# Kernel tuning notes

Hardware: AMD Instinct MI355X
Metric: run time of the kernel (lower is better)

The kernel has to match this reference:

```python
import jax, jax.numpy as jnp
import numpy as np

# Multi-scale feature pyramid (H, W) per level: strides 8/16/32/64 on a ~512px image
SHAPES = ((64, 64), (32, 32), (16, 16), (8, 8))
N_HEADS, N_LEVELS, N_POINTS = 8, 4, 4
D_MODEL = 256
HEAD_DIM = D_MODEL // N_HEADS


def setup_inputs() -> dict:
    key = jax.random.key(0)
    ks = jax.random.split(key, 11)
    B, C = 4, D_MODEL
    Lv = sum(h * w for h, w in SHAPES)  # 5440
    Lq = Lv  # encoder self-attention: queries are the flattened features
    scale = 0.02
    return {
        "query": jax.random.normal(ks[0], (B, Lq, C), jnp.float32),
        "reference_points": jax.random.uniform(ks[1], (B, Lq, N_LEVELS, 2), jnp.float32),
        "value": jax.random.normal(ks[2], (B, Lv, C), jnp.float32),
        "W_off": jax.random.normal(ks[3], (C, N_HEADS * N_LEVELS * N_POINTS * 2), jnp.float32) * scale,
        "b_off": jax.random.normal(ks[4], (N_HEADS * N_LEVELS * N_POINTS * 2,), jnp.float32) * 0.5,
        "W_attn": jax.random.normal(ks[5], (C, N_HEADS * N_LEVELS * N_POINTS), jnp.float32) * scale,
        "b_attn": jax.random.normal(ks[6], (N_HEADS * N_LEVELS * N_POINTS,), jnp.float32) * scale,
        "W_val": jax.random.normal(ks[7], (C, C), jnp.float32) * scale,
        "b_val": jax.random.normal(ks[8], (C,), jnp.float32) * scale,
        "W_out": jax.random.normal(ks[9], (C, C), jnp.float32) * scale,
        "b_out": jax.random.normal(ks[10], (C,), jnp.float32) * scale,
    }


def _bilinear_sample(val, grid, H, W):
    """Replicates F.grid_sample(mode='bilinear', padding_mode='zeros', align_corners=False).

    val:  [N, C, H, W]
    grid: [N, Lq, P, 2] in [-1, 1] (x, y order)
    returns: [N, C, Lq, P]
    """
    N, C = val.shape[0], val.shape[1]
    # unnormalize (align_corners=False)
    x = (grid[..., 0] + 1.0) * 0.5 * W - 0.5  # [N, Lq, P]
    y = (grid[..., 1] + 1.0) * 0.5 * H - 0.5
    x0 = jnp.floor(x)
    y0 = jnp.floor(y)
    wx = x - x0  # fractional parts
    wy = y - y0
    flat = val.reshape(N, C, H * W)

    def gather(xi, yi):
        valid = (xi >= 0) & (xi < W) & (yi >= 0) & (yi < H)
        xc = jnp.clip(xi, 0, W - 1).astype(jnp.int32)
        yc = jnp.clip(yi, 0, H - 1).astype(jnp.int32)
        idx = yc * W + xc  # [N, Lq, P]
        g = jax.vmap(lambda v, i: v[:, i])(flat, idx)  # [N, C, Lq, P]
        return g * valid[:, None, :, :].astype(val.dtype)

    out = (gather(x0, y0) * ((1 - wx) * (1 - wy))[:, None]
           + gather(x0 + 1, y0) * (wx * (1 - wy))[:, None]
           + gather(x0, y0 + 1) * ((1 - wx) * wy)[:, None]
           + gather(x0 + 1, y0 + 1) * (wx * wy)[:, None])
    return out


def _ms_deform_attn(query, reference_points, value, W_off, b_off, W_attn, b_attn,
                    W_val, b_val, W_out, b_out):
    B, Lq, C = query.shape
    val = value @ W_val + b_val  # [B, Lv, C]
    val = val.reshape(B, -1, N_HEADS, HEAD_DIM)

    offsets = (query @ W_off + b_off).reshape(B, Lq, N_HEADS, N_LEVELS, N_POINTS, 2)
    weights = jax.nn.softmax(
        (query @ W_attn + b_attn).reshape(B, Lq, N_HEADS, N_LEVELS * N_POINTS), axis=-1
    ).reshape(B, Lq, N_HEADS, N_LEVELS, N_POINTS)

    # offset normalizer: (W, H) per level
    offset_norm = jnp.array([[w, h] for h, w in SHAPES], jnp.float32)
    # ref_dim == 2 branch
    locs = reference_points[:, :, None, :, None, :] + offsets / offset_norm[None, None, None, :, None, :]
    grids = 2.0 * locs - 1.0  # [B, Lq, nh, nl, np, 2]

    acc = jnp.zeros((B * N_HEADS, HEAD_DIM, Lq), query.dtype)
    start = 0
    for lid, (H, W) in enumerate(SHAPES):
        # [B, HW, nh, hd] -> [B*nh, hd, H, W]
        v = val[:, start:start + H * W].transpose(0, 2, 3, 1).reshape(B * N_HEADS, HEAD_DIM, H, W)
        g = grids[:, :, :, lid].transpose(0, 2, 1, 3, 4).reshape(B * N_HEADS, Lq, N_POINTS, 2)
        s = _bilinear_sample(v, g, H, W)  # [B*nh, hd, Lq, np]
        w = weights[:, :, :, lid].transpose(0, 2, 1, 3).reshape(B * N_HEADS, 1, Lq, N_POINTS)
        acc = acc + (s * w).sum(-1)
        start += H * W

    out = acc.reshape(B, D_MODEL, Lq).transpose(0, 2, 1)  # [B, Lq, C]
    return out @ W_out + b_out


def reference(query, reference_points, value, W_off, b_off, W_attn, b_attn,
              W_val, b_val, W_out, b_out):
    return _ms_deform_attn(query, reference_points, value, W_off, b_off,
                           W_attn, b_attn, W_val, b_val, W_out, b_out)
```

## Files before the change

### kernel.cpp

```cpp
#include <hip/hip_runtime.h>


typedef __attribute__((ext_vector_type(8))) _Float16 half8;
typedef __attribute__((ext_vector_type(4))) _Float16 half4;
typedef __attribute__((ext_vector_type(4))) float f32x4;

typedef __attribute__((address_space(3))) unsigned int lds_uint;
typedef const __attribute__((address_space(1))) unsigned int g_uint;

__device__ __forceinline__ void load_lds16(const _Float16* g, _Float16* l) {
    __builtin_amdgcn_global_load_lds((g_uint*)g, (lds_uint*)l, 16, 0, 0);
}

__device__ __forceinline__ half8 splat8(_Float16 v) {
    half8 r = {v, v, v, v, v, v, v, v};
    return r;
}

#define M_TOTAL 21760

__global__ __launch_bounds__(256, 4) void gemm12_cvt(
    const float* __restrict__ value, const float* __restrict__ query,
    const float* __restrict__ W_val, const float* __restrict__ W_off,
    const float* __restrict__ W_attn,
    const float* __restrict__ b_val, const float* __restrict__ b_off,
    const float* __restrict__ b_attn,
    _Float16* __restrict__ valh, _Float16* __restrict__ offh)
{
    __shared__ _Float16 Af[2][4 * 64 * 8];
    __shared__ _Float16 Bf[2][4 * 128 * 8];

    const bool g1 = blockIdx.x < 680;
    const int id = g1 ? blockIdx.x : blockIdx.x - 680;
    const int mt = g1 ? (id >> 1) : (id / 3);
    const int nt = g1 ? (id & 1) : (id % 3);
    const int NN = g1 ? 256 : 384;
    const float* A = g1 ? value : query;
    _Float16* C = g1 ? valh : offh;
    const int bm = mt * 64;
    const int bn = nt * 128;

    const float* W;
    int sW, nb;
    if (g1)            { W = W_val;  sW = 256; nb = bn; }
    else if (nt < 2)   { W = W_off;  sW = 256; nb = bn; }
    else               { W = W_attn; sW = 128; nb = 0;  }

    const int tid = threadIdx.x;
    const int wave = tid >> 6, lane = tid & 63;
    const int wm = (wave & 1) * 32, wn = (wave >> 1) * 64;
    const int ml = lane & 15;
    const int gq = lane >> 4;

    const int ar = tid & 63,  ag = tid >> 6;
    const int bc = tid & 127, bh = tid >> 7;

    const float* aS = A + (size_t)(bm + ar) * 256 + ag * 8;
    const float* wS = W + (size_t)(bh * 16) * sW + nb + bc;

    float4 pa0, pa1;
    float pb[16];

    auto LOAD = [&](int kt) {
        const float* p = aS + kt * 32;
        pa0 = *(const float4*)(p + 0);
        pa1 = *(const float4*)(p + 4);
        const float* q = wS + (size_t)kt * 32 * sW;
#pragma unroll
        for (int e = 0; e < 16; ++e) pb[e] = q[(size_t)e * sW];
    };

    auto WRITE = [&](int buf) {
        const half8 ha = {(_Float16)pa0.x, (_Float16)pa0.y, (_Float16)pa0.z, (_Float16)pa0.w,
                          (_Float16)pa1.x, (_Float16)pa1.y, (_Float16)pa1.z, (_Float16)pa1.w};
        const half8 hb0 = {(_Float16)pb[0], (_Float16)pb[1], (_Float16)pb[2], (_Float16)pb[3],
                           (_Float16)pb[4], (_Float16)pb[5], (_Float16)pb[6], (_Float16)pb[7]};
        const half8 hb1 = {(_Float16)pb[8], (_Float16)pb[9], (_Float16)pb[10], (_Float16)pb[11],
                           (_Float16)pb[12], (_Float16)pb[13], (_Float16)pb[14], (_Float16)pb[15]};
        *(half8*)(&Af[buf][0] + ((ag * 64 + ar) << 3)) = ha;
        *(half8*)(&Bf[buf][0] + (((bh * 2) * 128 + bc) << 3)) = hb0;
        *(half8*)(&Bf[buf][0] + (((bh * 2 + 1) * 128 + bc) << 3)) = hb1;
    };

    const f32x4 zero4 = {0.f, 0.f, 0.f, 0.f};
    f32x4 acc[2][4];
#pragma unroll
    for (int i = 0; i < 2; ++i)
#pragma unroll
        for (int j = 0; j < 4; ++j) acc[i][j] = zero4;

    LOAD(0);
    int cur = 0;
    for (int kt = 0; kt < 8; ++kt) {
        WRITE(cur);
        if (kt < 7) LOAD(kt + 1);
        __syncthreads();

        half8 af[2], bf[4];
        const _Float16* ab = &Af[cur][0] + ((size_t)gq * 64 << 3);
        const _Float16* bb = &Bf[cur][0] + ((size_t)gq * 128 << 3);
#pragma unroll
        for (int i = 0; i < 2; ++i)
            af[i] = *(const half8*)(ab + ((wm + i * 16 + ml) << 3));
#pragma unroll
        for (int j = 0; j < 4; ++j)
            bf[j] = *(const half8*)(bb + ((wn + j * 16 + ml) << 3));
#pragma unroll
        for (int i = 0; i < 2; ++i)
#pragma unroll
            for (int j = 0; j < 4; ++j)
                acc[i][j] = __builtin_amdgcn_mfma_f32_16x16x32_f16(af[i], bf[j], acc[i][j], 0, 0, 0);
        cur ^= 1;
    }

    const int r0 = (lane >> 4) * 4;
#pragma unroll
    for (int j = 0; j < 4; ++j) {
        const int col = bn + wn + j * 16 + ml;
        const float bj = g1 ? b_val[col] : (col < 256 ? b_off[col] : b_attn[col - 256]);
#pragma unroll
        for (int i = 0; i < 2; ++i) {
            const size_t rbase = (size_t)(bm + wm + i * 16 + r0) * NN + col;
#pragma unroll
            for (int r = 0; r < 4; ++r)
                C[rbase + (size_t)r * NN] = (_Float16)(acc[i][j][r] + bj);
        }
    }
}

__device__ __forceinline__ void gemm_core(
    const _Float16* __restrict__ A, const _Float16* __restrict__ Bt,
    const float* __restrict__ bias, float* __restrict__ Cv,
    int NN, int mt, int nt)
{
    __shared__ _Float16 Ah[128 * 32];
    __shared__ _Float16 Bh[64 * 32];

    const int tid = threadIdx.x;
    const int bm = mt * 128;
    const int bn = nt * 64;
    const int wave = tid >> 6, lane = tid & 63;
    const int wm = (wave & 1) * 64, wn = (wave >> 1) * 32;
    const int ml = lane & 15, kq = (lane >> 4) * 8;
    const int lr = lane >> 2;
    const int lk = (lane & 3) * 8;

    const f32x4 zero4 = {0.f, 0.f, 0.f, 0.f};
    f32x4 acc[4][2];
#pragma unroll
    for (int i = 0; i < 4; ++i)
#pragma unroll
        for (int j = 0; j < 2; ++j) acc[i][j] = zero4;

    for (int kt = 0; kt < 8; ++kt) {
        const int k0 = kt * 32;
        __syncthreads();
#pragma unroll
        for (int t = 0; t < 2; ++t) {
            const int row = wave * 32 + t * 16;
            load_lds16(A + (size_t)(bm + row + lr) * 256 + k0 + lk,
                       Ah + (size_t)row * 32);
        }
        {
            const int row = wave * 16;
            load_lds16(Bt + (size_t)(bn + row + lr) * 256 + k0 + lk,
                       Bh + (size_t)row * 32);
        }
        __syncthreads();

        half8 af[4], bf[2];
#pragma unroll
        for (int i = 0; i < 4; ++i)
            af[i] = *(const half8*)(Ah + (wm + i * 16 + ml) * 32 + kq);
#pragma unroll
        for (int j = 0; j < 2; ++j)
            bf[j] = *(const half8*)(Bh + (wn + j * 16 + ml) * 32 + kq);
#pragma unroll
        for (int i = 0; i < 4; ++i)
#pragma unroll
            for (int j = 0; j < 2; ++j)
                acc[i][j] = __builtin_amdgcn_mfma_f32_16x16x32_f16(af[i], bf[j], acc[i][j], 0, 0, 0);
    }

    const int r0 = (lane >> 4) * 4;
#pragma unroll
    for (int j = 0; j < 2; ++j) {
        const int col = bn + wn + j * 16 + ml;
        const float bj = bias[col];
#pragma unroll
        for (int i = 0; i < 4; ++i) {
            const size_t rbase = (size_t)(bm + wm + i * 16 + r0) * NN + col;
#pragma unroll
            for (int r = 0; r < 4; ++r)
                Cv[rbase + (size_t)r * NN] = acc[i][j][r] + bj;
        }
    }
}

__global__ __launch_bounds__(256) void gemm_single(
    const _Float16* __restrict__ A, const _Float16* __restrict__ Bt,
    const float* __restrict__ bias, float* __restrict__ Cv)
{
    const int id = blockIdx.x;
    gemm_core(A, Bt, bias, Cv, 256, id >> 2, id & 3);
}

__global__ __launch_bounds__(256, 4) void sample_f16(
    const _Float16* __restrict__ valh,
    const float* __restrict__ refp,
    const _Float16* __restrict__ offh,
    const float* __restrict__ W_out,
    _Float16* __restrict__ wto,
    _Float16* __restrict__ acc_out)
{
    if (blockIdx.x < 256)
        wto[blockIdx.x * 256 + threadIdx.x] =
            (_Float16)W_out[threadIdx.x * 256 + blockIdx.x];

    const int wave = threadIdx.x >> 6, lane = threadIdx.x & 63;
    const int q2 = lane >> 5, sl = lane & 31;
    const int bq = blockIdx.x * 8 + wave * 2 + q2;
    const int b = bq / 5440;
    const int h = sl >> 2;
    const int t = sl & 3;
    const int d8 = t * 8;

    const int Wt = 64 >> t;
    const float fW = (float)Wt;

    const half8 ofr = *(const half8*)(offh + (size_t)bq * 384 + h * 32 + t * 8);
    const half4 lgt = *(const half4*)(offh + (size_t)bq * 384 + 256 + h * 16 + t * 4);
    const float2 rxy = *(const float2*)(refp + (size_t)bq * 8 + t * 2);

    float lg[4];
#pragma unroll
    for (int p = 0; p < 4; ++p) lg[p] = (float)lgt[p];

    float mx = fmaxf(fmaxf(lg[0], lg[1]), fmaxf(lg[2], lg[3]));
    mx = fmaxf(mx, __shfl_xor(mx, 1));
    mx = fmaxf(mx, __shfl_xor(mx, 2));
    float s = 0.f;
#pragma unroll
    for (int p = 0; p < 4; ++p) { lg[p] = __expf(lg[p] - mx); s += lg[p]; }
    s += __shfl_xor(s, 1);
    s += __shfl_xor(s, 2);
    const float inv = 1.f / s;

    unsigned pk[16];
#pragma unroll
    for (int p = 0; p < 4; ++p) {
        const float aw = lg[p] * inv;
        const float ox = (float)ofr[p * 2];
        const float oy = (float)ofr[p * 2 + 1];
        const float x = fmaf(rxy.x, fW, ox) - 0.5f;
        const float y = fmaf(rxy.y, fW, oy) - 0.5f;
        const float x0f = floorf(x), y0f = floorf(y);
        const int x0 = (int)x0f, y0 = (int)y0f;
        const float wx = x - x0f, wy = y - y0f;
        const bool okx0 = ((unsigned)x0 < (unsigned)Wt);
        const bool okx1 = ((unsigned)(x0 + 1) < (unsigned)Wt);
        const bool oky0 = ((unsigned)y0 < (unsigned)Wt);
        const bool oky1 = ((unsigned)(y0 + 1) < (unsigned)Wt);
        const int xc0 = min(max(x0, 0), Wt - 1);
        const int xc1 = min(max(x0 + 1, 0), Wt - 1);
        const int yc0 = min(max(y0, 0), Wt - 1);
        const int yc1 = min(max(y0 + 1, 0), Wt - 1);
        const _Float16 w0 = (_Float16)((okx0 & oky0) ? (1.f - wx) * (1.f - wy) * aw : 0.f);
        const _Float16 w1 = (_Float16)((okx1 & oky0) ? wx * (1.f - wy) * aw : 0.f);
        const _Float16 w2 = (_Float16)((okx0 & oky1) ? (1.f - wx) * wy * aw : 0.f);
        const _Float16 w3 = (_Float16)((okx1 & oky1) ? wx * wy * aw : 0.f);
        pk[p * 4 + 0] = ((unsigned)(yc0 * Wt + xc0) << 16) |
                        (unsigned)__builtin_bit_cast(unsigned short, w0);
        pk[p * 4 + 1] = ((unsigned)(yc0 * Wt + xc1) << 16) |
                        (unsigned)__builtin_bit_cast(unsigned short, w1);
        pk[p * 4 + 2] = ((unsigned)(yc1 * Wt + xc0) << 16) |
                        (unsigned)__builtin_bit_cast(unsigned short, w2);
        pk[p * 4 + 3] = ((unsigned)(yc1 * Wt + xc1) << 16) |
                        (unsigned)__builtin_bit_cast(unsigned short, w3);
    }

    const int starts_[4] = {0, 4096, 5120, 5376};
    const int gbase = lane & ~3;

    half8 acc = splat8((_Float16)0.f);
#pragma unroll
    for (int l = 0; l < 4; ++l) {
        const _Float16* vbase = valh + ((size_t)(b * 5440 + starts_[l])) * 256 + h * 32 + d8;
        const int src = gbase + l;

        unsigned q_[16];
#pragma unroll
        for (int c = 0; c < 16; ++c)
            q_[c] = (unsigned)__shfl((int)pk[c], src);

        __builtin_amdgcn_sched_barrier(0);
        half8 c_[16];
#pragma unroll
        for (int c = 0; c < 16; ++c)
            c_[c] = *(const half8*)(vbase + ((size_t)(q_[c] >> 16) << 8));
        __builtin_amdgcn_sched_barrier(0);
#pragma unroll
        for (int c = 0; c < 16; ++c)
            acc += c_[c] * splat8(__builtin_bit_cast(_Float16, (unsigned short)(q_[c] & 0xffffu)));
    }

    *(half8*)(acc_out + (size_t)bq * 256 + h * 32 + d8) = acc;
}

extern "C" void kernel_launch(void* const* d_in, const int* in_sizes, int n_in,
                              void* d_out, int out_size, void* d_ws, size_t ws_size,
                              hipStream_t stream) {
    const float* query  = (const float*)d_in[0];
    const float* refp   = (const float*)d_in[1];
    const float* value  = (const float*)d_in[2];
    const float* W_off  = (const float*)d_in[3];
    const float* b_off  = (const float*)d_in[4];
    const float* W_attn = (const float*)d_in[5];
    const float* b_attn = (const float*)d_in[6];
    const float* W_val  = (const float*)d_in[7];
    const float* b_val  = (const float*)d_in[8];
    const float* W_out  = (const float*)d_in[9];
    const float* b_out  = (const float*)d_in[10];
    float* out = (float*)d_out;

    const size_t M = M_TOTAL;

    _Float16* valh  = (_Float16*)d_ws;
    _Float16* offh  = valh + M * 256;
    _Float16* acc16 = offh + M * 384;
    _Float16* wto   = acc16 + M * 256;

    dim3 blk(256);
    gemm12_cvt<<<dim3(1700), blk, 0, stream>>>(
        value, query, W_val, W_off, W_attn, b_val, b_off, b_attn, valh, offh);
    sample_f16<<<dim3(M / 8), blk, 0, stream>>>(valh, refp, offh, W_out, wto, acc16);
    gemm_single<<<dim3(680), blk, 0, stream>>>(acc16, wto, b_out, out);
}
```

Before: 172.9 us.

## Pre-pack weights to fp16 tiles and load full K panels via direct LDS

Adds a small prep kernel that converts W_val, W_off and W_attn to fp16 in an MFMA-friendly packed layout. The projection GEMM now uses 64x64 tiles (twice as many blocks), loads the whole K=256 weight panel with global_load_lds and the whole A panel in one pass, then runs the MFMA loop without per-step syncs. This removes the strided fp32 weight loads and per-tile conversion in the GEMM, at the cost of an extra launch, more LDS per block (64 KB), and reloading A across more column tiles.

```diff
diff --git a/kernel.cpp b/kernel.cpp
--- a/kernel.cpp
+++ b/kernel.cpp
@@ -19,112 +19,100 @@
 
 #define M_TOTAL 21760
 
-__global__ __launch_bounds__(256, 4) void gemm12_cvt(
+__global__ __launch_bounds__(256) void prep_w(
+    const float* __restrict__ W_val, const float* __restrict__ W_off,
+    const float* __restrict__ W_attn, _Float16* __restrict__ wtf)
+{
+    const int slot = blockIdx.x * 256 + threadIdx.x;
+    const int T = slot >> 11;
+    const int rem = slot & 2047;
+    const int g = rem >> 6, nl = rem & 63;
+    half8 h;
+#pragma unroll
+    for (int e = 0; e < 8; ++e) {
+        const int k = g * 8 + e;
+        float v;
+        if (T < 4) {
+            v = W_val[k * 256 + T * 64 + nl];
+        } else {
+            const int n2 = (T - 4) * 64 + nl;
+            v = (n2 < 256) ? W_off[k * 256 + n2] : W_attn[k * 128 + (n2 - 256)];
+        }
+        h[e] = (_Float16)v;
+    }
+    *(half8*)(wtf + ((size_t)slot << 3)) = h;
+}
+
+__global__ __launch_bounds__(256) void gemm12_cvt(
     const float* __restrict__ value, const float* __restrict__ query,
-    const float* __restrict__ W_val, const float* __restrict__ W_off,
-    const float* __restrict__ W_attn,
+    const _Float16* __restrict__ wtf,
     const float* __restrict__ b_val, const float* __restrict__ b_off,
     const float* __restrict__ b_attn,
     _Float16* __restrict__ valh, _Float16* __restrict__ offh)
 {
-    __shared__ _Float16 Af[2][4 * 64 * 8];
-    __shared__ _Float16 Bf[2][4 * 128 * 8];
-
-    const bool g1 = blockIdx.x < 680;
-    const int id = g1 ? blockIdx.x : blockIdx.x - 680;
-    const int mt = g1 ? (id >> 1) : (id / 3);
-    const int nt = g1 ? (id & 1) : (id % 3);
+    __shared__ _Float16 Afs[32 * 64 * 8];
+    __shared__ _Float16 Bfs[32 * 64 * 8];
+
+    const bool g1 = blockIdx.x < 1360;
+    const int id = g1 ? blockIdx.x : blockIdx.x - 1360;
+    const int mt = g1 ? (id >> 2) : (id / 6);
+    const int nt = g1 ? (id & 3) : (id % 6);
     const int NN = g1 ? 256 : 384;
     const float* A = g1 ? value : query;
     _Float16* C = g1 ? valh : offh;
     const int bm = mt * 64;
-    const int bn = nt * 128;
-
-    const float* W;
-    int sW, nb;
-    if (g1)            { W = W_val;  sW = 256; nb = bn; }
-    else if (nt < 2)   { W = W_off;  sW = 256; nb = bn; }
-    else               { W = W_attn; sW = 128; nb = 0;  }
+    const int bn = nt * 64;
+    const int T  = g1 ? nt : 4 + nt;
 
     const int tid = threadIdx.x;
     const int wave = tid >> 6, lane = tid & 63;
-    const int wm = (wave & 1) * 32, wn = (wave >> 1) * 64;
-    const int ml = lane & 15;
-    const int gq = lane >> 4;
-
-    const int ar = tid & 63,  ag = tid >> 6;
-    const int bc = tid & 127, bh = tid >> 7;
-
-    const float* aS = A + (size_t)(bm + ar) * 256 + ag * 8;
-    const float* wS = W + (size_t)(bh * 16) * sW + nb + bc;
-
-    float4 pa0, pa1;
-    float pb[16];
-
-    auto LOAD = [&](int kt) {
-        const float* p = aS + kt * 32;
-        pa0 = *(const float4*)(p + 0);
-        pa1 = *(const float4*)(p + 4);
-        const float* q = wS + (size_t)kt * 32 * sW;
-#pragma unroll
-        for (int e = 0; e < 16; ++e) pb[e] = q[(size_t)e * sW];
-    };
-
-    auto WRITE = [&](int buf) {
-        const half8 ha = {(_Float16)pa0.x, (_Float16)pa0.y, (_Float16)pa0.z, (_Float16)pa0.w,
-                          (_Float16)pa1.x, (_Float16)pa1.y, (_Float16)pa1.z, (_Float16)pa1.w};
-        const half8 hb0 = {(_Float16)pb[0], (_Float16)pb[1], (_Float16)pb[2], (_Float16)pb[3],
-                           (_Float16)pb[4], (_Float16)pb[5], (_Float16)pb[6], (_Float16)pb[7]};
-        const half8 hb1 = {(_Float16)pb[8], (_Float16)pb[9], (_Float16)pb[10], (_Float16)pb[11],
-                           (_Float16)pb[12], (_Float16)pb[13], (_Float16)pb[14], (_Float16)pb[15]};
-        *(half8*)(&Af[buf][0] + ((ag * 64 + ar) << 3)) = ha;
-        *(half8*)(&Bf[buf][0] + (((bh * 2) * 128 + bc) << 3)) = hb0;
-        *(half8*)(&Bf[buf][0] + (((bh * 2 + 1) * 128 + bc) << 3)) = hb1;
-    };
+    const int ml = lane & 15, q = lane >> 4;
+
+    const _Float16* wsrc = wtf + ((size_t)T << 14);
+#pragma unroll
+    for (int i = 0; i < 8; ++i)
+        load_lds16(wsrc + (((size_t)i * 256 + tid) << 3),
+                   Bfs + (((size_t)i * 256 + wave * 64) << 3));
+
+    {
+        const int r = tid >> 2, c4 = tid & 3;
+        const float* ap = A + (size_t)(bm + r) * 256 + c4 * 64;
+        float4 pa[16];
+#pragma unroll
+        for (int j = 0; j < 16; ++j) pa[j] = *(const float4*)(ap + j * 4);
+#pragma unroll
+        for (int u = 0; u < 8; ++u) {
+            const float4 a0 = pa[2 * u], a1 = pa[2 * u + 1];
+            const half8 h = {(_Float16)a0.x, (_Float16)a0.y, (_Float16)a0.z, (_Float16)a0.w,
+                             (_Float16)a1.x, (_Float16)a1.y, (_Float16)a1.z, (_Float16)a1.w};
+            *(half8*)(Afs + (((c4 * 8 + u) * 64 + r) << 3)) = h;
+        }
+    }
+    __syncthreads();
 
     const f32x4 zero4 = {0.f, 0.f, 0.f, 0.f};
-    f32x4 acc[2][4];
-#pragma unroll
-    for (int i = 0; i < 2; ++i)
-#pragma unroll
-        for (int j = 0; j < 4; ++j) acc[i][j] = zero4;
-
-    LOAD(0);
-    int cur = 0;
+    f32x4 acc[4] = {zero4, zero4, zero4, zero4};
+
+#pragma unroll
     for (int kt = 0; kt < 8; ++kt) {
-        WRITE(cur);
-        if (kt < 7) LOAD(kt + 1);
-        __syncthreads();
-
-        half8 af[2], bf[4];
-        const _Float16* ab = &Af[cur][0] + ((size_t)gq * 64 << 3);
-        const _Float16* bb = &Bf[cur][0] + ((size_t)gq * 128 << 3);
-#pragma unroll
-        for (int i = 0; i < 2; ++i)
-            af[i] = *(const half8*)(ab + ((wm + i * 16 + ml) << 3));
-#pragma unroll
-        for (int j = 0; j < 4; ++j)
-            bf[j] = *(const half8*)(bb + ((wn + j * 16 + ml) << 3));
-#pragma unroll
-        for (int i = 0; i < 2; ++i)
-#pragma unroll
-            for (int j = 0; j < 4; ++j)
-                acc[i][j] = __builtin_amdgcn_mfma_f32_16x16x32_f16(af[i], bf[j], acc[i][j], 0, 0, 0);
-        cur ^= 1;
-    }
-
-    const int r0 = (lane >> 4) * 4;
+        const int g = kt * 4 + q;
+        const half8 af = *(const half8*)(Afs + (((size_t)g * 64 + wave * 16 + ml) << 3));
+#pragma unroll
+        for (int j = 0; j < 4; ++j) {
+            const half8 bf = *(const half8*)(Bfs + (((size_t)g * 64 + j * 16 + ml) << 3));
+            acc[j] = __builtin_amdgcn_mfma_f32_16x16x32_f16(af, bf, acc[j], 0, 0, 0);
+        }
+    }
+
+    const int r0 = q * 4;
 #pragma unroll
     for (int j = 0; j < 4; ++j) {
-        const int col = bn + wn + j * 16 + ml;
+        const int col = bn + j * 16 + ml;
         const float bj = g1 ? b_val[col] : (col < 256 ? b_off[col] : b_attn[col - 256]);
-#pragma unroll
-        for (int i = 0; i < 2; ++i) {
-            const size_t rbase = (size_t)(bm + wm + i * 16 + r0) * NN + col;
-#pragma unroll
-            for (int r = 0; r < 4; ++r)
-                C[rbase + (size_t)r * NN] = (_Float16)(acc[i][j][r] + bj);
-        }
+        const size_t rbase = (size_t)(bm + wave * 16 + r0) * NN + col;
+#pragma unroll
+        for (int r = 0; r < 4; ++r)
+            C[rbase + (size_t)r * NN] = (_Float16)(acc[j][r] + bj);
     }
 }
 
@@ -329,10 +317,12 @@
     _Float16* offh  = valh + M * 256;
     _Float16* acc16 = offh + M * 384;
     _Float16* wto   = acc16 + M * 256;
+    _Float16* wtf   = wto + 256 * 256;
 
     dim3 blk(256);
-    gemm12_cvt<<<dim3(1700), blk, 0, stream>>>(
-        value, query, W_val, W_off, W_attn, b_val, b_off, b_attn, valh, offh);
+    prep_w<<<dim3(80), blk, 0, stream>>>(W_val, W_off, W_attn, wtf);
+    gemm12_cvt<<<dim3(3400), blk, 0, stream>>>(
+        value, query, wtf, b_val, b_off, b_attn, valh, offh);
     sample_f16<<<dim3(M / 8), blk, 0, stream>>>(valh, refp, offh, W_out, wto, acc16);
     gemm_single<<<dim3(680), blk, 0, stream>>>(acc16, wto, b_out, out);
 }
```

After: 196.8 us. 13.8% more time.
